# Optimization experiments

Hardware: AMD Instinct MI355X
Metric: run time of the kernel (lower is better)

Reference implementation:

```python
import jax, jax.numpy as jnp
import numpy as np

S = 8192      # s: number of persons/nodes
F = 1024      # feature_len
A = 256       # attn_len
SIGMA_X, SIGMA_Y = 4.0, 1.0
EPS_VALID = 1e-8
EPS_DIS = 1e-4


def setup_inputs() -> dict:
    key = jax.random.key(0)
    ks = jax.random.split(key, 8)
    batch_data = jax.random.normal(ks[0], (S, F), dtype=jnp.float32)
    xywh = jax.random.uniform(ks[1], (S, 4), dtype=jnp.float32)  # positive -> all rows valid
    actor_weights = jax.random.uniform(ks[2], (S,), dtype=jnp.float32)
    avg_pos = jax.random.uniform(ks[3], (S, 2), dtype=jnp.float32)
    # learned params (kaiming-ish init, zero bias as in original)
    W_h = jax.random.normal(ks[4], (F, 2), dtype=jnp.float32) * (2.0 / F) ** 0.5
    b_h = jnp.zeros((2,), dtype=jnp.float32)
    W_g = jax.random.normal(ks[5], (F, A), dtype=jnp.float32) * (2.0 / F) ** 0.5
    b_g = jnp.zeros((A,), dtype=jnp.float32)
    return {
        "batch_data": batch_data, "xywh": xywh, "OW": 1920, "OH": 1080,
        "actor_weights": actor_weights, "avg_pos": avg_pos,
        "W_h": W_h, "b_h": b_h, "W_g": W_g, "b_g": b_g, "num_person": S,
    }


def reference(batch_data, xywh, OW, OH, actor_weights, avg_pos, W_h, b_h, W_g, b_g, num_person):
    # highlight_fc + tanh -> predicted offsets [S,2]
    hp = jnp.tanh(batch_data @ W_h + b_h)
    hx = hp[:, 0] * xywh[:, 2] * SIGMA_X + xywh[:, 0]  # [S]
    hy = hp[:, 1] * xywh[:, 3] * SIGMA_Y + xywh[:, 1]  # [S]

    # gcn_fc + relu -> node messages [S,A]
    targets = jax.nn.relu(batch_data @ W_g + b_g)

    # valid rows/cols: torch loop skips i/j with sum(xywh) < 1e-8
    valid = jnp.sum(xywh, axis=1) >= EPS_VALID  # [S] bool

    # pairwise inverse-distance weights [S,S] (the memory-bound core)
    dx = hx[:, None] - xywh[None, :, 0]
    dy = hy[:, None] - xywh[None, :, 1]
    dis = jnp.sqrt(dx * dx + dy * dy)
    pair_valid = valid[:, None] & valid[None, :]
    w = jnp.where(pair_valid, 1.0 / (dis + EPS_DIS), 0.0)
    row_sum = jnp.sum(w, axis=1, keepdims=True)
    w = jnp.where(valid[:, None], w / jnp.maximum(row_sum, 1e-30), 0.0)

    targets_weighted = w @ targets  # [S,A]
    return (targets_weighted, hp)
```

## Files before the change

kernel.cpp:

```cpp
#include <hip/hip_runtime.h>
#include <math.h>
#include <stdint.h>

typedef __attribute__((ext_vector_type(8))) short short8;
typedef __attribute__((ext_vector_type(4))) float f32x4;

__device__ __forceinline__ uint32_t cvt_pk_bf16(float lo, float hi) {
  uint32_t r;
  asm("v_cvt_pk_bf16_f32 %0, %1, %2" : "=v"(r) : "v"(lo), "v"(hi));
  return r;
}

__device__ __forceinline__ float wfun(float hx, float hy, float cx, float cy) {
  float dx = hx - cx, dy = hy - cy;
  float d = __builtin_amdgcn_sqrtf(fmaf(dx, dx, dy * dy));
  return __builtin_amdgcn_rcpf(d + 1e-4f);
}

__global__ __launch_bounds__(256) void k_head(
    const float* __restrict__ batch, const float* __restrict__ xywh,
    const float* __restrict__ W_h, const float* __restrict__ b_h,
    float* __restrict__ hp_out, float* __restrict__ hx, float* __restrict__ hy,
    float* __restrict__ validf, float2* __restrict__ cxy, int S, int F) {
  int wid = threadIdx.x >> 6;
  int lane = threadIdx.x & 63;
  int row = blockIdx.x * 4 + wid;
  if (row >= S) return;
  const float4* brow = (const float4*)(batch + (size_t)row * F);
  const float4* wh4 = (const float4*)W_h;
  int nf4 = F >> 2;
  float acc0 = 0.f, acc1 = 0.f;
  for (int k4 = lane; k4 < nf4; k4 += 64) {
    float4 b = brow[k4];
    float4 wa = wh4[2 * k4];
    float4 wb = wh4[2 * k4 + 1];
    acc0 += b.x * wa.x + b.y * wa.z + b.z * wb.x + b.w * wb.z;
    acc1 += b.x * wa.y + b.y * wa.w + b.z * wb.y + b.w * wb.w;
  }
  #pragma unroll
  for (int off = 32; off; off >>= 1) {
    acc0 += __shfl_xor(acc0, off, 64);
    acc1 += __shfl_xor(acc1, off, 64);
  }
  if (lane == 0) {
    float hp0 = tanhf(acc0 + b_h[0]);
    float hp1 = tanhf(acc1 + b_h[1]);
    float4 xy = ((const float4*)xywh)[row];
    hp_out[2 * row] = hp0;
    hp_out[2 * row + 1] = hp1;
    hx[row] = hp0 * xy.z * 4.0f + xy.x;
    hy[row] = hp1 * xy.w * 1.0f + xy.y;
    bool v = (xy.x + xy.y + xy.z + xy.w >= 1e-8f);
    validf[row] = v ? 1.0f : 0.0f;
    cxy[row] = v ? make_float2(xy.x, xy.y) : make_float2(1e30f, 1e30f);
  }
}

__global__ __launch_bounds__(256) void k_prep_w(
    const float* __restrict__ Wg, uint16_t* __restrict__ WgT, int F, int A) {
  int idx = blockIdx.x * 256 + threadIdx.x;
  int a = idx % A;
  int k0 = (idx / A) * 8;
  if (k0 >= F) return;
  float f[8];
  #pragma unroll
  for (int e = 0; e < 8; ++e) f[e] = Wg[(size_t)(k0 + e) * A + a];
  uint4 v;
  v.x = cvt_pk_bf16(f[0], f[1]);
  v.y = cvt_pk_bf16(f[2], f[3]);
  v.z = cvt_pk_bf16(f[4], f[5]);
  v.w = cvt_pk_bf16(f[6], f[7]);
  *(uint4*)(WgT + (size_t)a * F + k0) = v;
}

__global__ __launch_bounds__(256) void k_targets_mfma(
    const float* __restrict__ batch, const uint16_t* __restrict__ WgT,
    const float* __restrict__ bg, uint16_t* __restrict__ tgt2,
    int S, int F, int A) {
  int t = threadIdx.x;
  int lane = t & 63, wid = t >> 6;
  int wm = wid >> 1, wn = wid & 1;
  int i0 = blockIdx.x * 32;
  int row = i0 + wm * 16 + (lane & 15);
  int kch = lane >> 4;
  const float* ab = batch + (size_t)row * F + kch * 8;
  int ncol0 = wn * 128 + (lane & 15);
  const uint16_t* bb = WgT + (size_t)ncol0 * F + kch * 8;

  f32x4 acc[8] = {};
  float4 a0 = *(const float4*)(ab);
  float4 a1 = *(const float4*)(ab + 4);
  short8 bf[8];
  #pragma unroll
  for (int nf = 0; nf < 8; ++nf)
    bf[nf] = *(const short8*)(bb + (size_t)nf * 16 * F);

  for (int k0 = 0; k0 < F; k0 += 32) {
    int kn = (k0 + 32 < F) ? k0 + 32 : 0;
    float4 na0 = *(const float4*)(ab + kn);
    float4 na1 = *(const float4*)(ab + kn + 4);
    short8 nbf[8];
    #pragma unroll
    for (int nf = 0; nf < 8; ++nf)
      nbf[nf] = *(const short8*)(bb + kn + (size_t)nf * 16 * F);
    union { short8 s; uint32_t u[4]; } af;
    af.u[0] = cvt_pk_bf16(a0.x, a0.y);
    af.u[1] = cvt_pk_bf16(a0.z, a0.w);
    af.u[2] = cvt_pk_bf16(a1.x, a1.y);
    af.u[3] = cvt_pk_bf16(a1.z, a1.w);
    #pragma unroll
    for (int nf = 0; nf < 8; ++nf)
      acc[nf] = __builtin_amdgcn_mfma_f32_16x16x32_bf16(af.s, bf[nf], acc[nf], 0, 0, 0);
    a0 = na0; a1 = na1;
    #pragma unroll
    for (int nf = 0; nf < 8; ++nf) bf[nf] = nbf[nf];
  }

  int jb = blockIdx.x;
  int rloc = wm * 16 + (lane >> 4) * 4;
  #pragma unroll
  for (int nf = 0; nf < 8; ++nf) {
    int col = ncol0 + nf * 16;
    float b = bg[col];
    float o0 = fmaxf(acc[nf][0] + b, 0.f);
    float o1 = fmaxf(acc[nf][1] + b, 0.f);
    float o2 = fmaxf(acc[nf][2] + b, 0.f);
    float o3 = fmaxf(acc[nf][3] + b, 0.f);
    uint2 pk;
    pk.x = cvt_pk_bf16(o0, o1);
    pk.y = cvt_pk_bf16(o2, o3);
    *(uint2*)(tgt2 + ((size_t)jb * A + col) * 32 + rloc) = pk;
  }
}

__global__ __launch_bounds__(1024, 4) void k_gather_v8(
    const uint16_t* __restrict__ tgt2, const float2* __restrict__ cxy,
    const float* __restrict__ hx, const float* __restrict__ hy,
    const float* __restrict__ validf, float* __restrict__ out, int S, int A) {
  __shared__ uint16_t Bt[2][2][128][40];
  __shared__ float2  Ct[2][2][32];
  __shared__ float comb[64][132];
  __shared__ float rs2[2][64];
  __shared__ float scale_s[64];

  int t = threadIdx.x;
  int lane = t & 63, wid = t >> 6;
  int kg = wid >> 3;
  int sub = wid & 7;
  int wm = sub >> 1, wn = sub & 1;
  int colhalf = blockIdx.x;
  int i0 = blockIdx.y * 64;
  int mrow = i0 + wm * 16 + (lane & 15);
  int kch = lane >> 4;
  float hx_i = hx[mrow], hy_i = hy[mrow];
  int n0 = wn * 64 + (lane & 15);
  int nsteps = (S >> 1) / 32;
  const size_t TSTRIDE = (size_t)A * 32;

  int skg = t >> 9;
  int su = t & 511;
  int scol = su >> 2;
  int skw = su & 3;
  const uint16_t* gB0 = tgt2 + (size_t)(skg * nsteps) * TSTRIDE
                        + (size_t)colhalf * 128 * 32 + scol * 32 + skw * 8;
  const float2* gC0 = cxy + (size_t)(t >> 4) * (S >> 1) + (t & 15) * 2;

  f32x4 acc[4] = {};
  float rs = 0.f;

  {
    uint4 gb = *(const uint4*)(gB0);
    *(uint4*)&Bt[0][skg][scol][skw * 8] = gb;
    if (t < 32) {
      float4 gc = *(const float4*)(gC0);
      *(float4*)&Ct[0][t >> 4][(t & 15) * 2] = gc;
    }
  }
  __syncthreads();

  for (int ts = 0; ts < nsteps; ++ts) {
    int cur = ts & 1, nxt = cur ^ 1;
    int tn = (ts + 1 < nsteps) ? ts + 1 : 0;

    uint4 gb = *(const uint4*)(gB0 + (size_t)tn * TSTRIDE);
    float4 gc;
    if (t < 32) gc = *(const float4*)(gC0 + tn * 32);

    const float2* cp = &Ct[cur][kg][kch * 8];
    float4 c0 = *(const float4*)(cp);
    float4 c1 = *(const float4*)(cp + 2);
    float4 c2 = *(const float4*)(cp + 4);
    float4 c3 = *(const float4*)(cp + 6);

    short8 b0 = *(const short8*)&Bt[cur][kg][n0][kch * 8];
    short8 b1 = *(const short8*)&Bt[cur][kg][n0 + 16][kch * 8];
    short8 b2 = *(const short8*)&Bt[cur][kg][n0 + 32][kch * 8];
    short8 b3 = *(const short8*)&Bt[cur][kg][n0 + 48][kch * 8];

    float w0 = wfun(hx_i, hy_i, c0.x, c0.y);
    float w1 = wfun(hx_i, hy_i, c0.z, c0.w);
    float w2 = wfun(hx_i, hy_i, c1.x, c1.y);
    float w3 = wfun(hx_i, hy_i, c1.z, c1.w);
    float w4 = wfun(hx_i, hy_i, c2.x, c2.y);
    float w5 = wfun(hx_i, hy_i, c2.z, c2.w);
    float w6 = wfun(hx_i, hy_i, c3.x, c3.y);
    float w7 = wfun(hx_i, hy_i, c3.z, c3.w);
    rs += ((w0 + w1) + (w2 + w3)) + ((w4 + w5) + (w6 + w7));
    union { short8 s; uint32_t u[4]; } af;
    af.u[0] = cvt_pk_bf16(w0, w1);
    af.u[1] = cvt_pk_bf16(w2, w3);
    af.u[2] = cvt_pk_bf16(w4, w5);
    af.u[3] = cvt_pk_bf16(w6, w7);

    acc[0] = __builtin_amdgcn_mfma_f32_16x16x32_bf16(af.s, b0, acc[0], 0, 0, 0);
    acc[1] = __builtin_amdgcn_mfma_f32_16x16x32_bf16(af.s, b1, acc[1], 0, 0, 0);
    acc[2] = __builtin_amdgcn_mfma_f32_16x16x32_bf16(af.s, b2, acc[2], 0, 0, 0);
    acc[3] = __builtin_amdgcn_mfma_f32_16x16x32_bf16(af.s, b3, acc[3], 0, 0, 0);

    *(uint4*)&Bt[nxt][skg][scol][skw * 8] = gb;
    if (t < 32) *(float4*)&Ct[nxt][t >> 4][(t & 15) * 2] = gc;
    __syncthreads();
  }

  rs += __shfl_xor(rs, 16, 64);
  rs += __shfl_xor(rs, 32, 64);
  if (wn == 0 && lane < 16) rs2[kg][wm * 16 + lane] = rs;

  if (kg == 1) {
    int mre = wm * 16 + (lane >> 4) * 4;
    #pragma unroll
    for (int r = 0; r < 4; ++r) {
      comb[mre + r][n0]      = acc[0][r];
      comb[mre + r][n0 + 16] = acc[1][r];
      comb[mre + r][n0 + 32] = acc[2][r];
      comb[mre + r][n0 + 48] = acc[3][r];
    }
  }
  __syncthreads();
  if (t < 64) {
    float r = rs2[0][t] + rs2[1][t];
    float v = validf[i0 + t];
    scale_s[t] = (v > 0.f) ? 1.0f / fmaxf(r, 1e-30f) : 0.f;
  }
  __syncthreads();
  if (kg == 0) {
    int mre = wm * 16 + (lane >> 4) * 4;
    #pragma unroll
    for (int r = 0; r < 4; ++r) {
      float s = scale_s[mre + r];
      size_t base = (size_t)(i0 + mre + r) * A + colhalf * 128;
      out[base + n0]      = (acc[0][r] + comb[mre + r][n0]) * s;
      out[base + n0 + 16] = (acc[1][r] + comb[mre + r][n0 + 16]) * s;
      out[base + n0 + 32] = (acc[2][r] + comb[mre + r][n0 + 32]) * s;
      out[base + n0 + 48] = (acc[3][r] + comb[mre + r][n0 + 48]) * s;
    }
  }
}

extern "C" void kernel_launch(void* const* d_in, const int* in_sizes, int n_in,
                              void* d_out, int out_size, void* d_ws, size_t ws_size,
                              hipStream_t stream) {
  const float* batch = (const float*)d_in[0];
  const float* xywh  = (const float*)d_in[1];
  const float* W_h   = (const float*)d_in[6];
  const float* b_h   = (const float*)d_in[7];
  const float* W_g   = (const float*)d_in[8];
  const float* b_g   = (const float*)d_in[9];
  int S = in_sizes[4];
  int F = in_sizes[0] / S;
  int A = in_sizes[9];

  float* out    = (float*)d_out;
  float* out_tw = out;
  float* out_hp = out + (size_t)S * A;

  uint16_t* tgt2 = (uint16_t*)d_ws;
  uint16_t* WgT  = tgt2 + (size_t)A * S;
  float* hxv = (float*)(WgT + (size_t)A * F);
  float* hyv = hxv + S;
  float* vfv = hyv + S;
  float2* cxyv = (float2*)(vfv + S);

  k_head<<<dim3((S + 3) / 4), 256, 0, stream>>>(batch, xywh, W_h, b_h,
                                                out_hp, hxv, hyv, vfv, cxyv, S, F);
  k_prep_w<<<dim3((A * F / 8 + 255) / 256), 256, 0, stream>>>(W_g, WgT, F, A);
  k_targets_mfma<<<dim3(S / 32), 256, 0, stream>>>(batch, WgT, b_g, tgt2, S, F, A);
  k_gather_v8<<<dim3(2, S / 64), 1024, 0, stream>>>(tgt2, cxyv, hxv, hyv, vfv,
                                                    out_tw, S, A);
}
```

Measured before the change: 155.7 us.

## Split weight computation across wn waves and software-pipeline it via LDS

In the gather kernel, the two wn waves that share the same rows previously both computed all 8 pairwise weights per step. Now each computes half (4 weights), stages the packed bf16 A-fragment into LDS, and the weights for step t+1 are computed while the MFMAs for step t run. The loop is unrolled by two with explicit ping-pong buffers, the B tile row padding shrinks from 40 to 36, and row sums are combined across four partials. This halves the redundant sqrt/rcp work and overlaps it with the matrix ops, in exchange for an extra LDS write/read per step and a different bank-conflict pattern.

```diff
diff --git a/kernel.cpp b/kernel.cpp
--- a/kernel.cpp
+++ b/kernel.cpp
@@ -133,14 +133,14 @@
   }
 }
 
-__global__ __launch_bounds__(1024, 4) void k_gather_v8(
+__global__ __launch_bounds__(1024, 4) void k_gather_v9(
     const uint16_t* __restrict__ tgt2, const float2* __restrict__ cxy,
     const float* __restrict__ hx, const float* __restrict__ hy,
     const float* __restrict__ validf, float* __restrict__ out, int S, int A) {
-  __shared__ uint16_t Bt[2][2][128][40];
-  __shared__ float2  Ct[2][2][32];
+  __shared__ uint16_t Bt[2][2][128][36];
+  __shared__ uint32_t af_lds[2][2][4][64][4];
   __shared__ float comb[64][132];
-  __shared__ float rs2[2][64];
+  __shared__ float rs2[2][2][64];
   __shared__ float scale_s[64];
 
   int t = threadIdx.x;
@@ -161,70 +161,79 @@
   int su = t & 511;
   int scol = su >> 2;
   int skw = su & 3;
-  const uint16_t* gB0 = tgt2 + (size_t)(skg * nsteps) * TSTRIDE
+  const uint16_t* gBp = tgt2 + (size_t)(skg * nsteps) * TSTRIDE
                         + (size_t)colhalf * 128 * 32 + scol * 32 + skw * 8;
-  const float2* gC0 = cxy + (size_t)(t >> 4) * (S >> 1) + (t & 15) * 2;
+  const float2* gCp = cxy + (size_t)kg * (S >> 1) + kch * 8 + wn * 4;
 
   f32x4 acc[4] = {};
   float rs = 0.f;
 
+  uint16_t* btW0 = &Bt[0][skg][scol][skw * 8];
+  uint16_t* btW1 = &Bt[1][skg][scol][skw * 8];
+  uint32_t* afW0 = &af_lds[0][kg][wm][lane][wn * 2];
+  uint32_t* afW1 = &af_lds[1][kg][wm][lane][wn * 2];
+  const uint32_t* afR0 = &af_lds[0][kg][wm][lane][0];
+  const uint32_t* afR1 = &af_lds[1][kg][wm][lane][0];
+  const uint16_t* btR0 = &Bt[0][kg][n0][kch * 8];
+  const uint16_t* btR1 = &Bt[1][kg][n0][kch * 8];
+  const int COLS = 36;
+
   {
-    uint4 gb = *(const uint4*)(gB0);
-    *(uint4*)&Bt[0][skg][scol][skw * 8] = gb;
-    if (t < 32) {
-      float4 gc = *(const float4*)(gC0);
-      *(float4*)&Ct[0][t >> 4][(t & 15) * 2] = gc;
-    }
+    uint4 gb = *(const uint4*)gBp;  gBp += TSTRIDE;
+    float4 ca = *(const float4*)gCp;
+    float4 cb = *(const float4*)(gCp + 2);  gCp += 32;
+    float wA = wfun(hx_i, hy_i, ca.x, ca.y);
+    float wB = wfun(hx_i, hy_i, ca.z, ca.w);
+    float wC = wfun(hx_i, hy_i, cb.x, cb.y);
+    float wD = wfun(hx_i, hy_i, cb.z, cb.w);
+    rs += (wA + wB) + (wC + wD);
+    *(uint2*)afW0 = make_uint2(cvt_pk_bf16(wA, wB), cvt_pk_bf16(wC, wD));
+    *(uint4*)btW0 = gb;
   }
   __syncthreads();
 
-  for (int ts = 0; ts < nsteps; ++ts) {
-    int cur = ts & 1, nxt = cur ^ 1;
-    int tn = (ts + 1 < nsteps) ? ts + 1 : 0;
-
-    uint4 gb = *(const uint4*)(gB0 + (size_t)tn * TSTRIDE);
-    float4 gc;
-    if (t < 32) gc = *(const float4*)(gC0 + tn * 32);
-
-    const float2* cp = &Ct[cur][kg][kch * 8];
-    float4 c0 = *(const float4*)(cp);
-    float4 c1 = *(const float4*)(cp + 2);
-    float4 c2 = *(const float4*)(cp + 4);
-    float4 c3 = *(const float4*)(cp + 6);
-
-    short8 b0 = *(const short8*)&Bt[cur][kg][n0][kch * 8];
-    short8 b1 = *(const short8*)&Bt[cur][kg][n0 + 16][kch * 8];
-    short8 b2 = *(const short8*)&Bt[cur][kg][n0 + 32][kch * 8];
-    short8 b3 = *(const short8*)&Bt[cur][kg][n0 + 48][kch * 8];
-
-    float w0 = wfun(hx_i, hy_i, c0.x, c0.y);
-    float w1 = wfun(hx_i, hy_i, c0.z, c0.w);
-    float w2 = wfun(hx_i, hy_i, c1.x, c1.y);
-    float w3 = wfun(hx_i, hy_i, c1.z, c1.w);
-    float w4 = wfun(hx_i, hy_i, c2.x, c2.y);
-    float w5 = wfun(hx_i, hy_i, c2.z, c2.w);
-    float w6 = wfun(hx_i, hy_i, c3.x, c3.y);
-    float w7 = wfun(hx_i, hy_i, c3.z, c3.w);
-    rs += ((w0 + w1) + (w2 + w3)) + ((w4 + w5) + (w6 + w7));
-    union { short8 s; uint32_t u[4]; } af;
-    af.u[0] = cvt_pk_bf16(w0, w1);
-    af.u[1] = cvt_pk_bf16(w2, w3);
-    af.u[2] = cvt_pk_bf16(w4, w5);
-    af.u[3] = cvt_pk_bf16(w6, w7);
-
-    acc[0] = __builtin_amdgcn_mfma_f32_16x16x32_bf16(af.s, b0, acc[0], 0, 0, 0);
-    acc[1] = __builtin_amdgcn_mfma_f32_16x16x32_bf16(af.s, b1, acc[1], 0, 0, 0);
-    acc[2] = __builtin_amdgcn_mfma_f32_16x16x32_bf16(af.s, b2, acc[2], 0, 0, 0);
-    acc[3] = __builtin_amdgcn_mfma_f32_16x16x32_bf16(af.s, b3, acc[3], 0, 0, 0);
-
-    *(uint4*)&Bt[nxt][skg][scol][skw * 8] = gb;
-    if (t < 32) *(float4*)&Ct[nxt][t >> 4][(t & 15) * 2] = gc;
-    __syncthreads();
-  }
+#define GSTEP(AFR, BTR, AFW, BTW, DO_STAGE)                                    \
+  {                                                                            \
+    uint4 gb;                                                                  \
+    float4 ca, cb;                                                             \
+    if (DO_STAGE) {                                                            \
+      gb = *(const uint4*)gBp;  gBp += TSTRIDE;                                \
+      ca = *(const float4*)gCp;                                                \
+      cb = *(const float4*)(gCp + 2);  gCp += 32;                              \
+    }                                                                          \
+    short8 afr = *(const short8*)(AFR);                                        \
+    short8 b0 = *(const short8*)((BTR));                                       \
+    short8 b1 = *(const short8*)((BTR) + 16 * COLS);                           \
+    short8 b2 = *(const short8*)((BTR) + 32 * COLS);                           \
+    short8 b3 = *(const short8*)((BTR) + 48 * COLS);                           \
+    acc[0] = __builtin_amdgcn_mfma_f32_16x16x32_bf16(afr, b0, acc[0], 0, 0, 0);\
+    acc[1] = __builtin_amdgcn_mfma_f32_16x16x32_bf16(afr, b1, acc[1], 0, 0, 0);\
+    acc[2] = __builtin_amdgcn_mfma_f32_16x16x32_bf16(afr, b2, acc[2], 0, 0, 0);\
+    acc[3] = __builtin_amdgcn_mfma_f32_16x16x32_bf16(afr, b3, acc[3], 0, 0, 0);\
+    if (DO_STAGE) {                                                            \
+      float wA = wfun(hx_i, hy_i, ca.x, ca.y);                                 \
+      float wB = wfun(hx_i, hy_i, ca.z, ca.w);                                 \
+      float wC = wfun(hx_i, hy_i, cb.x, cb.y);                                 \
+      float wD = wfun(hx_i, hy_i, cb.z, cb.w);                                 \
+      rs += (wA + wB) + (wC + wD);                                             \
+      *(uint2*)(AFW) = make_uint2(cvt_pk_bf16(wA, wB), cvt_pk_bf16(wC, wD));   \
+      *(uint4*)(BTW) = gb;                                                     \
+    }                                                                          \
+    __syncthreads();                                                           \
+  }
+
+  int npairs = (nsteps >> 1) - 1;
+  for (int it = 0; it < npairs; ++it) {
+    GSTEP(afR0, btR0, afW1, btW1, true);
+    GSTEP(afR1, btR1, afW0, btW0, true);
+  }
+  GSTEP(afR0, btR0, afW1, btW1, true);
+  GSTEP(afR1, btR1, afW0, btW0, false);
+#undef GSTEP
 
   rs += __shfl_xor(rs, 16, 64);
   rs += __shfl_xor(rs, 32, 64);
-  if (wn == 0 && lane < 16) rs2[kg][wm * 16 + lane] = rs;
+  if (lane < 16) rs2[kg][wn][wm * 16 + lane] = rs;
 
   if (kg == 1) {
     int mre = wm * 16 + (lane >> 4) * 4;
@@ -238,7 +247,7 @@
   }
   __syncthreads();
   if (t < 64) {
-    float r = rs2[0][t] + rs2[1][t];
+    float r = (rs2[0][0][t] + rs2[0][1][t]) + (rs2[1][0][t] + rs2[1][1][t]);
     float v = validf[i0 + t];
     scale_s[t] = (v > 0.f) ? 1.0f / fmaxf(r, 1e-30f) : 0.f;
   }
@@ -285,6 +294,6 @@
                                                 out_hp, hxv, hyv, vfv, cxyv, S, F);
   k_prep_w<<<dim3((A * F / 8 + 255) / 256), 256, 0, stream>>>(W_g, WgT, F, A);
   k_targets_mfma<<<dim3(S / 32), 256, 0, stream>>>(batch, WgT, b_g, tgt2, S, F, A);
-  k_gather_v8<<<dim3(2, S / 64), 1024, 0, stream>>>(tgt2, cxyv, hxv, hyv, vfv,
+  k_gather_v9<<<dim3(2, S / 64), 1024, 0, stream>>>(tgt2, cxyv, hxv, hyv, vfv,
                                                     out_tw, S, A);
 }
```

Measured after the change: 353.2 us. 2.27x slower.
